# Kernel tuning notes

Measured on AMD Instinct MI355X. Metric: run time of the kernel, lower is better.

Reference implementation:

```python
import jax, jax.numpy as jnp
import numpy as np

D = 1024      # d_model
H = 16        # num_heads
DK = D // H   # head dim
L = 6         # num_layers
DFF = 4 * D   # feed-forward width
V = 32000     # vocab
B = 8         # batch
TP1 = 513     # target tokens (x length); decoded length = 512
S = 1024      # encoder frames
MAXLEN = 512
EPS = 1e-6


def make_pe(max_len, d):
    pos = np.arange(max_len, dtype=np.float64)[:, None]
    i = np.arange(0, d, 2, dtype=np.float64)[None, :]
    ang = pos / np.power(10000.0, i / d)
    pe = np.zeros((max_len, d), dtype=np.float32)
    pe[:, 0::2] = np.sin(ang)
    pe[:, 1::2] = np.cos(ang)
    return jnp.asarray(pe)


def setup_inputs() -> dict:
    key = jax.random.key(0)
    ks = jax.random.split(key, 16)
    sc = 0.02
    inp = {
        'x': jax.random.randint(ks[0], (B, TP1), 0, V, dtype=jnp.int64),
        'encoder_output': jax.random.normal(ks[1], (B, S, D), jnp.float32),
        'emb': jax.random.normal(ks[2], (V, D), jnp.float32) * sc,
        'pe': make_pe(MAXLEN, D),
        # per-layer stacked params; index 0..3 = q,k,v,out projections (in,out layout)
        'attn1_w': jax.random.normal(ks[3], (L, 4, D, D), jnp.float32) * sc,
        'attn1_b': jnp.zeros((L, 4, D), jnp.float32),
        'attn2_w': jax.random.normal(ks[4], (L, 4, D, D), jnp.float32) * sc,
        'attn2_b': jnp.zeros((L, 4, D), jnp.float32),
        'norm_a': jnp.ones((L, 3, D), jnp.float32),
        'norm_b': jnp.zeros((L, 3, D), jnp.float32),
        'ff1_w': jax.random.normal(ks[5], (L, D, DFF), jnp.float32) * sc,
        'ff1_b': jnp.zeros((L, DFF), jnp.float32),
        'ff2_w': jax.random.normal(ks[6], (L, DFF, D), jnp.float32) * sc,
        'ff2_b': jnp.zeros((L, D), jnp.float32),
        'fc_w': jax.random.normal(ks[7], (D, V), jnp.float32) * sc,
        'fc_b': jnp.zeros((V,), jnp.float32),
    }
    return inp


def _norm(x, a, b):
    mu = jnp.mean(x, axis=-1, keepdims=True)
    # torch .std() default is unbiased (ddof=1)
    var = jnp.sum((x - mu) ** 2, axis=-1, keepdims=True) / (x.shape[-1] - 1)
    return a * (x - mu) / (jnp.sqrt(var) + EPS) + b


def _mha(q_in, kv_in, w, b):
    # w: [4, D, D], b: [4, D]; masks in the original are no-ops (bug), omitted.
    bs, tq, _ = q_in.shape
    q = (q_in @ w[0] + b[0]).reshape(bs, tq, H, DK).transpose(0, 2, 1, 3)
    k = (kv_in @ w[1] + b[1]).reshape(bs, -1, H, DK).transpose(0, 2, 1, 3)
    v = (kv_in @ w[2] + b[2]).reshape(bs, -1, H, DK).transpose(0, 2, 1, 3)
    score = jnp.einsum('bhqd,bhkd->bhqk', q, k) / np.sqrt(DK).astype(np.float32)
    attn = jax.nn.softmax(score, axis=-1)
    o = jnp.einsum('bhqk,bhkd->bhqd', attn, v)
    o = o.transpose(0, 2, 1, 3).reshape(bs, tq, D)
    return o @ w[3] + b[3]


def reference(x, encoder_output, emb, pe, attn1_w, attn1_b, attn2_w, attn2_b,
              norm_a, norm_b, ff1_w, ff1_b, ff2_w, ff2_b, fc_w, fc_b):
    t = x.shape[1] - 1
    h = emb[x[:, :-1]] + pe[None, :t, :]  # [B, T, D]
    for l in range(L):
        a1 = _mha(h, h, attn1_w[l], attn1_b[l])
        h = _norm(a1 + h, norm_a[l, 0], norm_b[l, 0])
        a2 = _mha(h, encoder_output, attn2_w[l], attn2_b[l])
        h = _norm(a2 + h, norm_a[l, 1], norm_b[l, 1])
        f = jax.nn.relu(h @ ff1_w[l] + ff1_b[l]) @ ff2_w[l] + ff2_b[l]
        h = _norm(f + h, norm_a[l, 2], norm_b[l, 2])
    logits = h @ fc_w + fc_b  # [B, T, V]
    return jax.nn.log_softmax(logits, axis=-1)
```

## Files before the change

### kernel.cpp

```cpp
#include <hip/hip_runtime.h>

typedef __attribute__((ext_vector_type(4))) float f32x4;
typedef __attribute__((ext_vector_type(8))) __bf16 bfx8;
typedef unsigned short u16;
typedef unsigned int u32;

__device__ __forceinline__ u16 f2bf(float f) {
  u32 u = __builtin_bit_cast(u32, f);
  u = (u + 0x7FFFu + ((u >> 16) & 1u)) >> 16;
  return (u16)u;
}
__device__ __forceinline__ float bf2f(u16 u) {
  return __builtin_bit_cast(float, ((u32)u) << 16);
}

typedef __attribute__((address_space(1))) const void gvoid;
typedef __attribute__((address_space(3))) void svoid;
__device__ __forceinline__ void gload16(const void* g, void* l) {
  __builtin_amdgcn_global_load_lds((gvoid*)g, (svoid*)l, 16, 0, 0);
}

__device__ __forceinline__ float wredsum(float v) {
#pragma unroll
  for (int o = 32; o; o >>= 1) v += __shfl_xor(v, o, 64);
  return v;
}
__device__ __forceinline__ float wredmax(float v) {
#pragma unroll
  for (int o = 32; o; o >>= 1) v = fmaxf(v, __shfl_xor(v, o, 64));
  return v;
}

__global__ __launch_bounds__(256) void wconv_kernel(const float* __restrict__ in,
                                                    u16* __restrict__ out, int K, int N) {
  __shared__ u16 tile[32][33];
  const long z = blockIdx.z;
  const float* iz = in + z * (long)K * N;
  u16* oz = out + z * (long)K * N;
  const int n0 = blockIdx.x << 5, k0 = blockIdx.y << 5;
  const int tx = threadIdx.x & 31, ty = threadIdx.x >> 5;
#pragma unroll
  for (int i = 0; i < 4; ++i)
    tile[ty + 8 * i][tx] = f2bf(iz[(long)(k0 + ty + 8 * i) * N + n0 + tx]);
  __syncthreads();
#pragma unroll
  for (int i = 0; i < 4; ++i)
    oz[(long)(n0 + ty + 8 * i) * K + k0 + tx] = tile[tx][ty + 8 * i];
}

__global__ __launch_bounds__(256) void cvt_kernel(const float* __restrict__ in,
                                                  u16* __restrict__ out, long n) {
  long i = ((long)blockIdx.x * 256 + threadIdx.x) * 4;
  if (i + 3 < n) {
    float4 v = *(const float4*)(in + i);
    ushort4 o = {f2bf(v.x), f2bf(v.y), f2bf(v.z), f2bf(v.w)};
    *(ushort4*)(out + i) = o;
  }
}

__global__ __launch_bounds__(256) void embed_kernel(const int* __restrict__ x,
                                                    const float* __restrict__ emb,
                                                    const float* __restrict__ pe,
                                                    float* __restrict__ h,
                                                    u16* __restrict__ hb) {
  const int row = blockIdx.x;
  const int b = row >> 9, t = row & 511;
  const long tok = (long)x[b * 513 + t];
  const int d = threadIdx.x << 2;
  float4 e = *(const float4*)(emb + tok * 1024 + d);
  float4 p = *(const float4*)(pe + (long)t * 1024 + d);
  float4 v = {e.x + p.x, e.y + p.y, e.z + p.z, e.w + p.w};
  *(float4*)(h + (long)row * 1024 + d) = v;
  ushort4 o = {f2bf(v.x), f2bf(v.y), f2bf(v.z), f2bf(v.w)};
  *(ushort4*)(hb + (long)row * 1024 + d) = o;
}

__global__ __launch_bounds__(256) void addnorm_kernel(const float* __restrict__ delta,
                                                      const float* __restrict__ delta2,
                                                      float* __restrict__ h,
                                                      u16* __restrict__ hb,
                                                      const float* __restrict__ ga,
                                                      const float* __restrict__ gb) {
  __shared__ float r1[4], r2[4];
  const long row = blockIdx.x;
  const int d = threadIdx.x << 2;
  float4 a = *(const float4*)(h + row * 1024 + d);
  float4 q = *(const float4*)(delta + row * 1024 + d);
  float4 q2 = *(const float4*)(delta2 + row * 1024 + d);
  float x0 = a.x + q.x + q2.x, x1 = a.y + q.y + q2.y;
  float x2 = a.z + q.z + q2.z, x3 = a.w + q.w + q2.w;
  float s1 = wredsum(x0 + x1 + x2 + x3);
  float s2 = wredsum(x0 * x0 + x1 * x1 + x2 * x2 + x3 * x3);
  if ((threadIdx.x & 63) == 0) { r1[threadIdx.x >> 6] = s1; r2[threadIdx.x >> 6] = s2; }
  __syncthreads();
  float S1 = r1[0] + r1[1] + r1[2] + r1[3];
  float S2 = r2[0] + r2[1] + r2[2] + r2[3];
  float mu = S1 * (1.0f / 1024.0f);
  float var = (S2 - S1 * mu) * (1.0f / 1023.0f);
  float inv = 1.0f / (sqrtf(fmaxf(var, 0.f)) + 1e-6f);
  float4 g4 = *(const float4*)(ga + d);
  float4 b4 = *(const float4*)(gb + d);
  float y0 = g4.x * (x0 - mu) * inv + b4.x;
  float y1 = g4.y * (x1 - mu) * inv + b4.y;
  float y2 = g4.z * (x2 - mu) * inv + b4.z;
  float y3 = g4.w * (x3 - mu) * inv + b4.w;
  float4 y = {y0, y1, y2, y3};
  *(float4*)(h + row * 1024 + d) = y;
  ushort4 o = {f2bf(y0), f2bf(y1), f2bf(y2), f2bf(y3)};
  *(ushort4*)(hb + row * 1024 + d) = o;
}

__global__ __launch_bounds__(256) void logsoftmax_kernel(float* __restrict__ lg) {
  const long row = blockIdx.x;
  float* lr = lg + row * 32000L;
  float m = -1e30f, s = 0.f;
  for (int j = threadIdx.x; j < 8000; j += 256) {
    float4 v = *(const float4*)(lr + (long)j * 4);
    float lm = fmaxf(fmaxf(v.x, v.y), fmaxf(v.z, v.w));
    if (lm > m) { s *= __expf(m - lm); m = lm; }
    s += __expf(v.x - m) + __expf(v.y - m) + __expf(v.z - m) + __expf(v.w - m);
  }
#pragma unroll
  for (int o = 32; o; o >>= 1) {
    float om = __shfl_xor(m, o, 64), os = __shfl_xor(s, o, 64);
    float M = fmaxf(m, om);
    s = s * __expf(m - M) + os * __expf(om - M);
    m = M;
  }
  __shared__ float rm[4], rs[4];
  if ((threadIdx.x & 63) == 0) { rm[threadIdx.x >> 6] = m; rs[threadIdx.x >> 6] = s; }
  __syncthreads();
  float M = fmaxf(fmaxf(rm[0], rm[1]), fmaxf(rm[2], rm[3]));
  float S = rs[0] * __expf(rm[0] - M) + rs[1] * __expf(rm[1] - M) +
            rs[2] * __expf(rm[2] - M) + rs[3] * __expf(rm[3] - M);
  float lse = M + __logf(S);
  for (int j = threadIdx.x; j < 8000; j += 256) {
    float4 v = *(const float4*)(lr + (long)j * 4);
    v.x -= lse; v.y -= lse; v.z -= lse; v.w -= lse;
    *(float4*)(lr + (long)j * 4) = v;
  }
}

__global__ __launch_bounds__(512) void logsoftmax_bf16_kernel(const u16* __restrict__ lg,
                                                              float* __restrict__ out) {
  __shared__ u16 rl[32000];
  __shared__ float rr[8];
  const long row = blockIdx.x;
  const u16* lr = lg + row * 32000L;
  float* od = out + row * 32000L;
  const int tid = threadIdx.x;
  float m0 = -1e30f, m1 = -1e30f;
  for (int j = tid * 8; j < 32000; j += 4096) {
    ushort4 a = *(const ushort4*)(lr + j);
    ushort4 b = *(const ushort4*)(lr + j + 4);
    *(ushort4*)&rl[j] = a;
    *(ushort4*)&rl[j + 4] = b;
    m0 = fmaxf(m0, fmaxf(fmaxf(bf2f(a.x), bf2f(a.y)), fmaxf(bf2f(a.z), bf2f(a.w))));
    m1 = fmaxf(m1, fmaxf(fmaxf(bf2f(b.x), bf2f(b.y)), fmaxf(bf2f(b.z), bf2f(b.w))));
  }
  float m = wredmax(fmaxf(m0, m1));
  if ((tid & 63) == 0) rr[tid >> 6] = m;
  __syncthreads();
  m = fmaxf(fmaxf(fmaxf(rr[0], rr[1]), fmaxf(rr[2], rr[3])),
            fmaxf(fmaxf(rr[4], rr[5]), fmaxf(rr[6], rr[7])));
  __syncthreads();
  float s0 = 0.f, s1 = 0.f;
  for (int j = tid * 8; j < 32000; j += 4096) {
    ushort4 a = *(const ushort4*)&rl[j];
    ushort4 b = *(const ushort4*)&rl[j + 4];
    s0 += __expf(bf2f(a.x) - m) + __expf(bf2f(a.y) - m) +
          __expf(bf2f(a.z) - m) + __expf(bf2f(a.w) - m);
    s1 += __expf(bf2f(b.x) - m) + __expf(bf2f(b.y) - m) +
          __expf(bf2f(b.z) - m) + __expf(bf2f(b.w) - m);
  }
  float s = wredsum(s0 + s1);
  if ((tid & 63) == 0) rr[tid >> 6] = s;
  __syncthreads();
  s = rr[0] + rr[1] + rr[2] + rr[3] + rr[4] + rr[5] + rr[6] + rr[7];
  const float lse = m + __logf(s);
  for (int j = tid * 8; j < 32000; j += 4096) {
    ushort4 a = *(const ushort4*)&rl[j];
    ushort4 b = *(const ushort4*)&rl[j + 4];
    float4 o0 = {bf2f(a.x) - lse, bf2f(a.y) - lse, bf2f(a.z) - lse, bf2f(a.w) - lse};
    float4 o1 = {bf2f(b.x) - lse, bf2f(b.y) - lse, bf2f(b.z) - lse, bf2f(b.w) - lse};
    *(float4*)(od + j) = o0;
    *(float4*)(od + j + 4) = o1;
  }
}

template <int SKV>
__global__ __launch_bounds__(512) void attn_kernel(const u16* __restrict__ Q,
                                                   const u16* __restrict__ Kb,
                                                   const u16* __restrict__ Vt,
                                                   u16* __restrict__ ctx) {
  __shared__ u16 Kl[2][4096];
  __shared__ u16 Vl[2][4096];
  __shared__ u16 Pl[8][16][72];
  const int tid = threadIdx.x, lane = tid & 63, wave = tid >> 6;
  const int l15 = lane & 15, lg = lane >> 4;
  const int bh = blockIdx.y;
  const int qrow = blockIdx.x * 128 + wave * 16 + l15;
  const u16* qp = Q + ((long)bh * 512 + qrow) * 64 + lg * 8;
  bfx8 qf0 = *(const bfx8*)(qp);
  bfx8 qf1 = *(const bfx8*)(qp + 32);

  const int srow = tid >> 3;
  const int schunk = (tid & 7) ^ (srow & 7);
  const u16* Kbb = Kb + ((long)bh * SKV + srow) * 64 + schunk * 8;
  const u16* Vtb2 = Vt + ((long)bh * 64 + srow) * SKV + schunk * 8;

  auto stage = [&](int t, int buf) {
    const int kv0 = t * 64;
    gload16(Kbb + (long)kv0 * 64, &Kl[buf][tid * 8]);
    gload16(Vtb2 + kv0, &Vl[buf][tid * 8]);
  };

  const f32x4 zf = {0.f, 0.f, 0.f, 0.f};
  f32x4 acc_o[4] = {zf, zf, zf, zf};
  float mrun = -1e30f, lrun = 0.f;
  const int swk = l15 & 7;
  constexpr int NT = SKV / 64;

  stage(0, 0);
  __syncthreads();
  int buf = 0;
#pragma unroll 1
  for (int t = 0; t < NT; ++t) {
    if (t + 1 < NT) stage(t + 1, buf ^ 1);
    f32x4 sacc[4];
#pragma unroll
    for (int kvt = 0; kvt < 4; ++kvt) {
      const int krow = kvt * 16 + l15;
      bfx8 kf0 = *(const bfx8*)&Kl[buf][krow * 64 + ((lg ^ swk) << 3)];
      bfx8 kf1 = *(const bfx8*)&Kl[buf][krow * 64 + (((4 + lg) ^ swk) << 3)];
      f32x4 tt = __builtin_amdgcn_mfma_f32_16x16x32_bf16(kf0, qf0, zf, 0, 0, 0);
      sacc[kvt] = __builtin_amdgcn_mfma_f32_16x16x32_bf16(kf1, qf1, tt, 0, 0, 0);
    }
    float pm = -1e30f;
#pragma unroll
    for (int kvt = 0; kvt < 4; ++kvt)
#pragma unroll
      for (int r = 0; r < 4; ++r) pm = fmaxf(pm, sacc[kvt][r]);
    pm = fmaxf(pm, __shfl_xor(pm, 16, 64));
    pm = fmaxf(pm, __shfl_xor(pm, 32, 64));
    pm *= 0.125f;
    const bool grow = !__all(pm <= mrun);
    const float mnew = grow ? fmaxf(mrun, pm) : mrun;
    float psum = 0.f;
#pragma unroll
    for (int kvt = 0; kvt < 4; ++kvt)
#pragma unroll
      for (int r = 0; r < 4; ++r) {
        float p = __expf(sacc[kvt][r] * 0.125f - mnew);
        psum += p;
        Pl[wave][l15][kvt * 16 + lg * 4 + r] = f2bf(p);
      }
    psum += __shfl_xor(psum, 16, 64);
    psum += __shfl_xor(psum, 32, 64);
    if (grow) {
      const float corr = __expf(mrun - mnew);
      lrun = lrun * corr + psum;
      mrun = mnew;
#pragma unroll
      for (int dt = 0; dt < 4; ++dt) {
        acc_o[dt][0] *= corr; acc_o[dt][1] *= corr;
        acc_o[dt][2] *= corr; acc_o[dt][3] *= corr;
      }
    } else {
      lrun += psum;
    }
    bfx8 pf0 = *(const bfx8*)&Pl[wave][l15][lg * 8];
    bfx8 pf1 = *(const bfx8*)&Pl[wave][l15][32 + lg * 8];
#pragma unroll
    for (int dt = 0; dt < 4; ++dt) {
      const int vrow = dt * 16 + l15;
      bfx8 vf0 = *(const bfx8*)&Vl[buf][vrow * 64 + ((lg ^ swk) << 3)];
      bfx8 vf1 = *(const bfx8*)&Vl[buf][vrow * 64 + (((4 + lg) ^ swk) << 3)];
      acc_o[dt] = __builtin_amdgcn_mfma_f32_16x16x32_bf16(vf0, pf0, acc_o[dt], 0, 0, 0);
      acc_o[dt] = __builtin_amdgcn_mfma_f32_16x16x32_bf16(vf1, pf1, acc_o[dt], 0, 0, 0);
    }
    __syncthreads();
    buf ^= 1;
  }
  const float inv = 1.0f / lrun;
  const int b = bh >> 4, hh = bh & 15;
  u16* crow = ctx + ((long)b * 512 + qrow) * 1024 + hh * 64;
#pragma unroll
  for (int dt = 0; dt < 4; ++dt)
#pragma unroll
    for (int r = 0; r < 4; ++r)
      crow[dt * 16 + lg * 4 + r] = f2bf(acc_o[dt][r] * inv);
}

template <int BM, int BN, int WMW, int WNW, int EPI, bool RELU>
__global__ __launch_bounds__(256) void gemm_bt(const u16* __restrict__ A, long sAz, int lda,
                                               const u16* __restrict__ Bt, long sBz, int ldb,
                                               const float* __restrict__ bias,
                                               void* __restrict__ out, long sCz, int ldc,
                                               int K, int Ttok) {
  constexpr int WROWS = BM / WMW, WCOLS = BN / WNW;
  constexpr int MI = WROWS / 16, NI = WCOLS / 16;
  __shared__ u16 As[BM * 32];
  __shared__ u16 Bs[BN * 32];
  const int tid = threadIdx.x, lane = tid & 63, wave = tid >> 6;
  const int l15 = lane & 15, lg = lane >> 4;
  const int wm = wave / WNW, wn = wave % WNW;
  const int bx = blockIdx.x, by = blockIdx.y;
  const long z = blockIdx.z;
  const int srow = tid >> 2, scol = (tid & 3) << 3;
  const u16* Aa = A + z * sAz + (long)(by * BM + srow) * lda + scol;
  const u16* Ba = Bt + z * sBz + (long)(bx * BN + srow) * ldb + scol;

  f32x4 acc[MI][NI];
#pragma unroll
  for (int i = 0; i < MI; ++i)
#pragma unroll
    for (int j = 0; j < NI; ++j) acc[i][j] = (f32x4){0.f, 0.f, 0.f, 0.f};

  for (int kt = 0; kt < K; kt += 32) {
#pragma unroll
    for (int i = 0; i < BM / 64; ++i)
      gload16(Aa + (long)i * 64 * lda + kt, &As[i * 2048 + tid * 8]);
#pragma unroll
    for (int i = 0; i < BN / 64; ++i)
      gload16(Ba + (long)i * 64 * ldb + kt, &Bs[i * 2048 + tid * 8]);
    __syncthreads();
    bfx8 afr[MI], bfr[NI];
#pragma unroll
    for (int i = 0; i < MI; ++i)
      afr[i] = *(const bfx8*)&As[(wm * WROWS + i * 16 + l15) * 32 + (lg << 3)];
#pragma unroll
    for (int j = 0; j < NI; ++j)
      bfr[j] = *(const bfx8*)&Bs[(wn * WCOLS + j * 16 + l15) * 32 + (lg << 3)];
#pragma unroll
    for (int i = 0; i < MI; ++i)
#pragma unroll
      for (int j = 0; j < NI; ++j)
        acc[i][j] = __builtin_amdgcn_mfma_f32_16x16x32_bf16(afr[i], bfr[j], acc[i][j], 0, 0, 0);
    __syncthreads();
  }

  const int gm0 = by * BM + wm * WROWS;
  const int gn0 = bx * BN + wn * WCOLS;
#pragma unroll
  for (int i = 0; i < MI; ++i) {
#pragma unroll
    for (int j = 0; j < NI; ++j) {
      const int gn = gn0 + j * 16 + l15;
      const float bv = (bias && z == 0) ? bias[gn] : 0.f;
#pragma unroll
      for (int r = 0; r < 4; ++r) {
        const int gm = gm0 + i * 16 + (lg << 2) + r;
        float v = acc[i][j][r] + bv;
        if (RELU) v = fmaxf(v, 0.f);
        if constexpr (EPI == 0) {
          ((float*)out)[z * sCz + (long)gm * ldc + gn] = v;
        } else if constexpr (EPI == 1) {
          ((u16*)out)[z * sCz + (long)gm * ldc + gn] = f2bf(v);
        } else if constexpr (EPI == 3) {
          const int b = gm / Ttok, t = gm - b * Ttok;
          const int hh = gn >> 6, dk = gn & 63;
          ((u16*)out)[(((long)(b * 16 + hh) * Ttok + t) << 6) + dk] = f2bf(v);
        }
      }
    }
  }
}

#define MMAQ(hm, hn)                                                                   \
  {                                                                                    \
    _Pragma("unroll") for (int kk = 0; kk < 2; ++kk)                                   \
        _Pragma("unroll") for (int i = 0; i < 4; ++i)                                  \
            _Pragma("unroll") for (int jn = 0; jn < 2; ++jn)                           \
                acc[(hm)*4 + i][(hn)*2 + jn] = __builtin_amdgcn_mfma_f32_16x16x32_bf16( \
                    a[i][kk], b[jn][kk], acc[(hm)*4 + i][(hn)*2 + jn], 0, 0, 0);       \
  }

template <int EPI, bool RELU>
__global__ __launch_bounds__(512, 2) void gemm256(const u16* __restrict__ A, int lda,
                                                  const u16* __restrict__ Bt, int ldb,
                                                  const float* __restrict__ bias,
                                                  void* __restrict__ out, int ldc, int K,
                                                  int Ttok, void* __restrict__ out2,
                                                  void* __restrict__ out3, int gx) {
  __shared__ u16 lds[2][2][2][8192];
  const int tid = threadIdx.x, lane = tid & 63;
  const int wid = tid >> 6, wm = wid >> 2, wn = wid & 3;
  const int l15 = lane & 15, lg = lane >> 4;
  const int S = gx >> 3;
  const int xcd = blockIdx.x & 7, idx = blockIdx.x >> 3;
  const int mt = xcd * S + idx % S;
  const int nt_ = idx / S;
  const int NT = K >> 6;

  const int r0 = tid >> 3;
  const int blkx = (tid & 7) ^ (r0 & 7);
  const u16* Abase = A + (long)(mt * 256 + r0) * lda + blkx * 8;
  const u16* Bbase = Bt + (long)(nt_ * 256 + r0) * ldb + blkx * 8;

  auto stageA = [&](int s, int half) {
    const int kts = (s < NT ? s : NT - 1) << 6;
    const u16* g = Abase + (long)(half * 128) * lda + kts;
    gload16(g, &lds[s & 1][0][half][tid * 8]);
    gload16(g + (long)64 * lda, &lds[s & 1][0][half][(512 + tid) * 8]);
  };
  auto stageB = [&](int s, int half) {
    const int kts = (s < NT ? s : NT - 1) << 6;
    const u16* g = Bbase + (long)(half * 128) * ldb + kts;
    gload16(g, &lds[s & 1][1][half][tid * 8]);
    gload16(g + (long)64 * ldb, &lds[s & 1][1][half][(512 + tid) * 8]);
  };

  f32x4 acc[8][4];
#pragma unroll
  for (int i = 0; i < 8; ++i)
#pragma unroll
    for (int j = 0; j < 4; ++j) acc[i][j] = (f32x4){0.f, 0.f, 0.f, 0.f};
  bfx8 a[4][2], b[2][2];

  const int sw = l15 & 7;
  auto loadA = [&](int buf, int hm) {
#pragma unroll
    for (int i = 0; i < 4; ++i) {
      const int row = hm * 64 + i * 16 + l15;
#pragma unroll
      for (int kk = 0; kk < 2; ++kk)
        a[i][kk] = *(const bfx8*)&lds[buf][0][wm][row * 64 + (((kk * 4 + lg) ^ sw) << 3)];
    }
  };
  auto loadB = [&](int buf, int hn) {
#pragma unroll
    for (int jn = 0; jn < 2; ++jn) {
      const int row = (wn & 1) * 64 + hn * 32 + jn * 16 + l15;
#pragma unroll
      for (int kk = 0; kk < 2; ++kk)
        b[jn][kk] = *(const bfx8*)&lds[buf][1][wn >> 1][row * 64 + (((kk * 4 + lg) ^ sw) << 3)];
    }
  };

  stageA(0, 0); stageA(0, 1); stageB(0, 0); stageB(0, 1);
  stageA(1, 0); stageA(1, 1);
  asm volatile("s_waitcnt vmcnt(4)" ::: "memory");
  __builtin_amdgcn_s_barrier();

  for (int t = 0; t < NT; ++t) {
    const int p = t & 1;
    loadA(p, 0); loadB(p, 0);
    stageB(t + 1, 0);
    __builtin_amdgcn_s_barrier();
    asm volatile("s_waitcnt lgkmcnt(0)" ::: "memory");
    __builtin_amdgcn_s_setprio(1);
    MMAQ(0, 0);
    __builtin_amdgcn_s_setprio(0);
    __builtin_amdgcn_s_barrier();
    loadB(p, 1);
    stageB(t + 1, 1);
    __builtin_amdgcn_s_barrier();
    asm volatile("s_waitcnt lgkmcnt(0)" ::: "memory");
    __builtin_amdgcn_s_setprio(1);
    MMAQ(0, 1);
    __builtin_amdgcn_s_setprio(0);
    __builtin_amdgcn_s_barrier();
    loadA(p, 1); loadB(p, 0);
    stageA(t + 2, 0);
    __builtin_amdgcn_s_barrier();
    asm volatile("s_waitcnt lgkmcnt(0)" ::: "memory");
    __builtin_amdgcn_s_setprio(1);
    MMAQ(1, 0);
    __builtin_amdgcn_s_setprio(0);
    __builtin_amdgcn_s_barrier();
    loadB(p, 1);
    stageA(t + 2, 1);
    asm volatile("s_waitcnt vmcnt(4)" ::: "memory");
    __builtin_amdgcn_s_barrier();
    asm volatile("s_waitcnt lgkmcnt(0)" ::: "memory");
    __builtin_amdgcn_s_setprio(1);
    MMAQ(1, 1);
    __builtin_amdgcn_s_setprio(0);
    __builtin_amdgcn_s_barrier();
  }

  const int gm0 = mt * 256 + wm * 128;
  const int gn0 = nt_ * 256 + wn * 64;
#pragma unroll
  for (int ii = 0; ii < 8; ++ii) {
#pragma unroll
    for (int jj = 0; jj < 4; ++jj) {
      const int gn = gn0 + jj * 16 + l15;
      const float bv = bias ? bias[gn] : 0.f;
#pragma unroll
      for (int r = 0; r < 4; ++r) {
        const int gm = gm0 + ii * 16 + (lg << 2) + r;
        float v = acc[ii][jj][r] + bv;
        if (RELU) v = fmaxf(v, 0.f);
        if constexpr (EPI == 0) {
          ((float*)out)[(long)gm * ldc + gn] = v;
        } else if constexpr (EPI == 1) {
          ((u16*)out)[(long)gm * ldc + gn] = f2bf(v);
        } else if constexpr (EPI == 6) {
          const int bq = gm / Ttok, t2 = gm - bq * Ttok;
          const int sec = gn >> 10, w1 = gn & 1023;
          const int hh = w1 >> 6, dk = w1 & 63;
          const u16 val = f2bf(v);
          if (sec == 0)
            ((u16*)out)[(((long)(bq * 16 + hh) * Ttok + t2) << 6) + dk] = val;
          else if (sec == 1)
            ((u16*)out2)[(((long)(bq * 16 + hh) * Ttok + t2) << 6) + dk] = val;
          else
            ((u16*)out3)[((long)((bq * 16 + hh) << 6) + dk) * Ttok + t2] = val;
        } else if constexpr (EPI == 7) {
          const int bq = gm / Ttok, t2 = gm - bq * Ttok;
          const int sec = gn >> 10, w1 = gn & 1023;
          const int hh = w1 >> 6, dk = w1 & 63;
          const u16 val = f2bf(v);
          if (sec == 0)
            ((u16*)out)[(((long)(bq * 16 + hh) * Ttok + t2) << 6) + dk] = val;
          else
            ((u16*)out2)[((long)((bq * 16 + hh) << 6) + dk) * Ttok + t2] = val;
        }
      }
    }
  }
}

extern "C" void kernel_launch(void* const* d_in, const int* in_sizes, int n_in,
                              void* d_out, int out_size, void* d_ws, size_t ws_size,
                              hipStream_t stream) {
  const int* x = (const int*)d_in[0];
  const float* enc = (const float*)d_in[1];
  const float* emb = (const float*)d_in[2];
  const float* pe = (const float*)d_in[3];
  const float* a1w = (const float*)d_in[4];
  const float* a1b = (const float*)d_in[5];
  const float* a2w = (const float*)d_in[6];
  const float* a2b = (const float*)d_in[7];
  const float* nra = (const float*)d_in[8];
  const float* nrb = (const float*)d_in[9];
  const float* f1w = (const float*)d_in[10];
  const float* f1b = (const float*)d_in[11];
  const float* f2w = (const float*)d_in[12];
  const float* f2b = (const float*)d_in[13];
  const float* fcw = (const float*)d_in[14];
  const float* fcb = (const float*)d_in[15];
  float* out = (float*)d_out;

  char* base = (char*)d_ws;
  size_t off = 0;
  auto alloc = [&](size_t bytes) -> void* {
    void* p = base + off;
    off += (bytes + 255) & ~(size_t)255;
    return p;
  };
  const long wsz = 1024 * 1024;
  const bool big = ws_size >= (600ull << 20);
  u16* wT = (u16*)alloc(96ull * wsz * 2);
  u16* encb = (u16*)alloc(8ull * wsz * 2);
  float* h = (float*)alloc(4ull * wsz * 4);
  u16* hb = (u16*)alloc(4ull * wsz * 2);
  u16* qb = (u16*)alloc(4ull * wsz * 2);
  u16* kb = (u16*)alloc(8ull * wsz * 2);
  u16* vtb = (u16*)alloc(8ull * wsz * 2);
  u16* ctxb = (u16*)alloc(4ull * wsz * 2);
  float* af = (float*)alloc(4ull * wsz * 4);
  float* af2 = (float*)alloc(4ull * wsz * 4);
  u16* midb = (u16*)alloc(16ull * wsz * 2);
  u16* fcT = qb;
  u16* lgb = big ? (u16*)alloc(4096ull * 32000 * 2) : nullptr;

  u16* wTa1 = wT;
  u16* wTa2 = wT + 24 * wsz;
  u16* wTf1 = wT + 48 * wsz;
  u16* wTf2 = wT + 72 * wsz;

  cvt_kernel<<<dim3(8192), dim3(256), 0, stream>>>(enc, encb, 8ll * wsz);
  embed_kernel<<<dim3(4096), dim3(256), 0, stream>>>(x, emb, pe, h, hb);
  wconv_kernel<<<dim3(32, 32, 24), dim3(256), 0, stream>>>(a1w, wTa1, 1024, 1024);
  wconv_kernel<<<dim3(32, 32, 24), dim3(256), 0, stream>>>(a2w, wTa2, 1024, 1024);
  wconv_kernel<<<dim3(128, 32, 6), dim3(256), 0, stream>>>(f1w, wTf1, 1024, 4096);
  wconv_kernel<<<dim3(32, 128, 6), dim3(256), 0, stream>>>(f2w, wTf2, 4096, 1024);

  for (int l = 0; l < 6; ++l) {
    const float* b1 = a1b + (long)l * 4096;
    const float* b2 = a2b + (long)l * 4096;
    const u16* w1 = wTa1 + (long)l * 4 * wsz;
    const u16* w2 = wTa2 + (long)l * 4 * wsz;

    gemm256<6, false><<<dim3(192), dim3(512), 0, stream>>>(
        hb, 1024, w1, 1024, b1, qb, 0, 1024, 512, kb, vtb, 16);
    attn_kernel<512><<<dim3(4, 128), dim3(512), 0, stream>>>(qb, kb, vtb, ctxb);
    gemm_bt<128, 128, 2, 2, 0, false><<<dim3(8, 32, 2), dim3(256), 0, stream>>>(
        ctxb, 512, 1024, w1 + 3 * wsz, 512, 1024, b1 + 3072, af, 4194304, 1024, 512, 0);
    addnorm_kernel<<<dim3(4096), dim3(256), 0, stream>>>(
        af, af2, h, hb, nra + (l * 3 + 0) * 1024, nrb + (l * 3 + 0) * 1024);

    gemm_bt<64, 128, 2, 2, 3, false><<<dim3(8, 64, 1), dim3(256), 0, stream>>>(
        hb, 0, 1024, w2, 0, 1024, b2, qb, 0, 0, 1024, 512);
    gemm256<7, false><<<dim3(256), dim3(512), 0, stream>>>(
        encb, 1024, w2 + wsz, 1024, b2 + 1024, kb, 0, 1024, 1024, vtb, nullptr, 32);
    attn_kernel<1024><<<dim3(4, 128), dim3(512), 0, stream>>>(qb, kb, vtb, ctxb);
    gemm_bt<128, 128, 2, 2, 0, false><<<dim3(8, 32, 2), dim3(256), 0, stream>>>(
        ctxb, 512, 1024, w2 + 3 * wsz, 512, 1024, b2 + 3072, af, 4194304, 1024, 512, 0);
    addnorm_kernel<<<dim3(4096), dim3(256), 0, stream>>>(
        af, af2, h, hb, nra + (l * 3 + 1) * 1024, nrb + (l * 3 + 1) * 1024);

    gemm256<1, true><<<dim3(256), dim3(512), 0, stream>>>(
        hb, 1024, wTf1 + (long)l * 4 * wsz, 1024, f1b + (long)l * 4096, midb, 4096, 1024, 0,
        nullptr, nullptr, 16);
    gemm_bt<128, 128, 2, 2, 0, false><<<dim3(8, 32, 2), dim3(256), 0, stream>>>(
        midb, 2048, 4096, wTf2 + (long)l * 4 * wsz, 2048, 4096, f2b + (long)l * 1024, af,
        4194304, 1024, 2048, 0);
    addnorm_kernel<<<dim3(4096), dim3(256), 0, stream>>>(
        af, af2, h, hb, nra + (l * 3 + 2) * 1024, nrb + (l * 3 + 2) * 1024);
  }

  wconv_kernel<<<dim3(1000, 32, 1), dim3(256), 0, stream>>>(fcw, fcT, 1024, 32000);
  if (big) {
    gemm256<1, false><<<dim3(2000), dim3(512), 0, stream>>>(
        hb, 1024, fcT, 1024, fcb, lgb, 32000, 1024, 0, nullptr, nullptr, 16);
    logsoftmax_bf16_kernel<<<dim3(4096), dim3(512), 0, stream>>>(lgb, out);
  } else {
    gemm256<0, false><<<dim3(2000), dim3(512), 0, stream>>>(
        hb, 1024, fcT, 1024, fcb, out, 32000, 1024, 0, nullptr, nullptr, 16);
    logsoftmax_kernel<<<dim3(4096), dim3(256), 0, stream>>>(out);
  }
}
```

Before: 3.088 ms.

## Batch cross-attention K/V projections for all layers into one GEMM; prioritize attention MFMAs

Because the encoder output is the same for every layer, the cross-attention K and V projections for all six layers are computed up front in a single large GEMM. A new BMAP row mapping selects the K/V weight rows and biases, and a new epilogue scatters results into per-layer K and V^T buffers. This replaces six smaller per-layer launches with one larger launch that fills the GPU better. The per-layer K/V storage reuses the logits scratch buffer, so it only runs when enough workspace is available. The attention kernel also raises wave priority around its MFMA sections.

```diff
diff --git a/kernel.cpp b/kernel.cpp
--- a/kernel.cpp
+++ b/kernel.cpp
@@ -228,6 +228,7 @@
   for (int t = 0; t < NT; ++t) {
     if (t + 1 < NT) stage(t + 1, buf ^ 1);
     f32x4 sacc[4];
+    __builtin_amdgcn_s_setprio(1);
 #pragma unroll
     for (int kvt = 0; kvt < 4; ++kvt) {
       const int krow = kvt * 16 + l15;
@@ -236,6 +237,7 @@
       f32x4 tt = __builtin_amdgcn_mfma_f32_16x16x32_bf16(kf0, qf0, zf, 0, 0, 0);
       sacc[kvt] = __builtin_amdgcn_mfma_f32_16x16x32_bf16(kf1, qf1, tt, 0, 0, 0);
     }
+    __builtin_amdgcn_s_setprio(0);
     float pm = -1e30f;
 #pragma unroll
     for (int kvt = 0; kvt < 4; ++kvt)
@@ -271,6 +273,7 @@
     }
     bfx8 pf0 = *(const bfx8*)&Pl[wave][l15][lg * 8];
     bfx8 pf1 = *(const bfx8*)&Pl[wave][l15][32 + lg * 8];
+    __builtin_amdgcn_s_setprio(1);
 #pragma unroll
     for (int dt = 0; dt < 4; ++dt) {
       const int vrow = dt * 16 + l15;
@@ -279,6 +282,7 @@
       acc_o[dt] = __builtin_amdgcn_mfma_f32_16x16x32_bf16(vf0, pf0, acc_o[dt], 0, 0, 0);
       acc_o[dt] = __builtin_amdgcn_mfma_f32_16x16x32_bf16(vf1, pf1, acc_o[dt], 0, 0, 0);
     }
+    __builtin_amdgcn_s_setprio(0);
     __syncthreads();
     buf ^= 1;
   }
@@ -376,7 +380,7 @@
                     a[i][kk], b[jn][kk], acc[(hm)*4 + i][(hn)*2 + jn], 0, 0, 0);       \
   }
 
-template <int EPI, bool RELU>
+template <int EPI, bool RELU, int BMAP>
 __global__ __launch_bounds__(512, 2) void gemm256(const u16* __restrict__ A, int lda,
                                                   const u16* __restrict__ Bt, int ldb,
                                                   const float* __restrict__ bias,
@@ -395,8 +399,14 @@
 
   const int r0 = tid >> 3;
   const int blkx = (tid & 7) ^ (r0 & 7);
+  const int n0 = nt_ * 256;
+  long brow0;
+  if constexpr (BMAP == 1)
+    brow0 = (long)(n0 >> 11) * 4096 + 1024 + (n0 & 2047);
+  else
+    brow0 = n0;
   const u16* Abase = A + (long)(mt * 256 + r0) * lda + blkx * 8;
-  const u16* Bbase = Bt + (long)(nt_ * 256 + r0) * ldb + blkx * 8;
+  const u16* Bbase = Bt + (brow0 + r0) * ldb + blkx * 8;
 
   auto stageA = [&](int s, int half) {
     const int kts = (s < NT ? s : NT - 1) << 6;
@@ -487,7 +497,11 @@
 #pragma unroll
     for (int jj = 0; jj < 4; ++jj) {
       const int gn = gn0 + jj * 16 + l15;
-      const float bv = bias ? bias[gn] : 0.f;
+      float bv;
+      if constexpr (BMAP == 1)
+        bv = bias[(gn >> 11) * 4096 + 1024 + (gn & 2047)];
+      else
+        bv = bias ? bias[gn] : 0.f;
 #pragma unroll
       for (int r = 0; r < 4; ++r) {
         const int gm = gm0 + ii * 16 + (lg << 2) + r;
@@ -517,6 +531,16 @@
             ((u16*)out)[(((long)(bq * 16 + hh) * Ttok + t2) << 6) + dk] = val;
           else
             ((u16*)out2)[((long)((bq * 16 + hh) << 6) + dk) * Ttok + t2] = val;
+        } else if constexpr (EPI == 8) {
+          const int l = gn >> 11, inner = gn & 2047;
+          const int sec = inner >> 10, w1 = inner & 1023;
+          const int hh = w1 >> 6, dk = w1 & 63;
+          const int bq = gm >> 10, t2 = gm & 1023;
+          const u16 val = f2bf(v);
+          if (sec == 0)
+            ((u16*)out)[((((long)l * 8 + bq) * 16 + hh) * 1024 + t2) * 64 + dk] = val;
+          else
+            ((u16*)out2)[((((long)l * 8 + bq) * 16 + hh) * 64 + dk) * 1024 + t2] = val;
         }
       }
     }
@@ -565,7 +589,10 @@
   float* af2 = (float*)alloc(4ull * wsz * 4);
   u16* midb = (u16*)alloc(16ull * wsz * 2);
   u16* fcT = qb;
-  u16* lgb = big ? (u16*)alloc(4096ull * 32000 * 2) : nullptr;
+  u16* kv6 = big ? (u16*)alloc(262144000) : nullptr;
+  u16* kb6 = kv6;
+  u16* vtb6 = kv6 ? kv6 + 50331648 : nullptr;
+  u16* lgb = kv6;
 
   u16* wTa1 = wT;
   u16* wTa2 = wT + 24 * wsz;
@@ -579,13 +606,18 @@
   wconv_kernel<<<dim3(128, 32, 6), dim3(256), 0, stream>>>(f1w, wTf1, 1024, 4096);
   wconv_kernel<<<dim3(32, 128, 6), dim3(256), 0, stream>>>(f2w, wTf2, 4096, 1024);
 
+  if (big) {
+    gemm256<8, false, 1><<<dim3(1536), dim3(512), 0, stream>>>(
+        encb, 1024, wTa2, 1024, a2b, kb6, 0, 1024, 1024, vtb6, nullptr, 32);
+  }
+
   for (int l = 0; l < 6; ++l) {
     const float* b1 = a1b + (long)l * 4096;
     const float* b2 = a2b + (long)l * 4096;
     const u16* w1 = wTa1 + (long)l * 4 * wsz;
     const u16* w2 = wTa2 + (long)l * 4 * wsz;
 
-    gemm256<6, false><<<dim3(192), dim3(512), 0, stream>>>(
+    gemm256<6, false, 0><<<dim3(192), dim3(512), 0, stream>>>(
         hb, 1024, w1, 1024, b1, qb, 0, 1024, 512, kb, vtb, 16);
     attn_kernel<512><<<dim3(4, 128), dim3(512), 0, stream>>>(qb, kb, vtb, ctxb);
     gemm_bt<128, 128, 2, 2, 0, false><<<dim3(8, 32, 2), dim3(256), 0, stream>>>(
@@ -595,15 +627,24 @@
 
     gemm_bt<64, 128, 2, 2, 3, false><<<dim3(8, 64, 1), dim3(256), 0, stream>>>(
         hb, 0, 1024, w2, 0, 1024, b2, qb, 0, 0, 1024, 512);
-    gemm256<7, false><<<dim3(256), dim3(512), 0, stream>>>(
-        encb, 1024, w2 + wsz, 1024, b2 + 1024, kb, 0, 1024, 1024, vtb, nullptr, 32);
-    attn_kernel<1024><<<dim3(4, 128), dim3(512), 0, stream>>>(qb, kb, vtb, ctxb);
+    const u16* lK;
+    const u16* lV;
+    if (big) {
+      lK = kb6 + (long)l * 8388608;
+      lV = vtb6 + (long)l * 8388608;
+    } else {
+      gemm256<7, false, 0><<<dim3(256), dim3(512), 0, stream>>>(
+          encb, 1024, w2 + wsz, 1024, b2 + 1024, kb, 0, 1024, 1024, vtb, nullptr, 32);
+      lK = kb;
+      lV = vtb;
+    }
+    attn_kernel<1024><<<dim3(4, 128), dim3(512), 0, stream>>>(qb, lK, lV, ctxb);
     gemm_bt<128, 128, 2, 2, 0, false><<<dim3(8, 32, 2), dim3(256), 0, stream>>>(
         ctxb, 512, 1024, w2 + 3 * wsz, 512, 1024, b2 + 3072, af, 4194304, 1024, 512, 0);
     addnorm_kernel<<<dim3(4096), dim3(256), 0, stream>>>(
         af, af2, h, hb, nra + (l * 3 + 1) * 1024, nrb + (l * 3 + 1) * 1024);
 
-    gemm256<1, true><<<dim3(256), dim3(512), 0, stream>>>(
+    gemm256<1, true, 0><<<dim3(256), dim3(512), 0, stream>>>(
         hb, 1024, wTf1 + (long)l * 4 * wsz, 1024, f1b + (long)l * 4096, midb, 4096, 1024, 0,
         nullptr, nullptr, 16);
     gemm_bt<128, 128, 2, 2, 0, false><<<dim3(8, 32, 2), dim3(256), 0, stream>>>(
@@ -615,11 +656,11 @@
 
   wconv_kernel<<<dim3(1000, 32, 1), dim3(256), 0, stream>>>(fcw, fcT, 1024, 32000);
   if (big) {
-    gemm256<1, false><<<dim3(2000), dim3(512), 0, stream>>>(
+    gemm256<1, false, 0><<<dim3(2000), dim3(512), 0, stream>>>(
         hb, 1024, fcT, 1024, fcb, lgb, 32000, 1024, 0, nullptr, nullptr, 16);
     logsoftmax_bf16_kernel<<<dim3(4096), dim3(512), 0, stream>>>(lgb, out);
   } else {
-    gemm256<0, false><<<dim3(2000), dim3(512), 0, stream>>>(
+    gemm256<0, false, 0><<<dim3(2000), dim3(512), 0, stream>>>(
         hb, 1024, fcT, 1024, fcb, out, 32000, 1024, 0, nullptr, nullptr, 16);
     logsoftmax_kernel<<<dim3(4096), dim3(256), 0, stream>>>(out);
   }
```

Measured after the change: 3.031 ms. No clear change (-1.8%).
